# Kernel optimization log

Hardware: AMD Instinct MI355X
Metric: run time of the kernel (lower is better)

The kernel has to match this reference:

```python
import jax, jax.numpy as jnp
import numpy as np

B, S, DA, DV, DU, L, M = 16, 256, 1, 32, 1, 4, 12


def conv1x1(x, w, b):
    # x: [B,C,H,W], w: [O,C], b: [O]
    return jnp.einsum('bchw,oc->bohw', x, w) + b[None, :, None, None]


def setup_inputs() -> dict:
    key = jax.random.key(0)
    ks = jax.random.split(key, 12)
    sc = 0.02
    return {
        'x':    jax.random.normal(ks[0], (B, S, S, DA), dtype=jnp.float32),
        'p_w':  sc * jax.random.normal(ks[1], (DV, DA + 2), dtype=jnp.float32),
        'p_b':  sc * jax.random.normal(ks[2], (DV,), dtype=jnp.float32),
        'ws_w': sc * jax.random.normal(ks[3], (L, DV, DV), dtype=jnp.float32),
        'ws_b': sc * jax.random.normal(ks[4], (L, DV), dtype=jnp.float32),
        'w1r':  sc * jax.random.normal(ks[5], (L, DV, DV, M, M), dtype=jnp.float32),
        'w1i':  sc * jax.random.normal(ks[6], (L, DV, DV, M, M), dtype=jnp.float32),
        'w2r':  sc * jax.random.normal(ks[7], (L, DV, DV, M, M), dtype=jnp.float32),
        'w2i':  sc * jax.random.normal(ks[8], (L, DV, DV, M, M), dtype=jnp.float32),
        'q_w':  sc * jax.random.normal(ks[9], (DU, DV), dtype=jnp.float32),
        'q_b':  sc * jax.random.normal(ks[10], (DU,), dtype=jnp.float32),
    }


def fourier_layer(x, w1r, w1i, w2r, w2i):
    # x: [B,C,H,W]; FFT norm None == 'backward' (numpy/jax default)
    b, c, h, w = x.shape
    x_ft = jnp.fft.rfft2(x)                       # [B,C,H,W//2+1] complex
    W1 = w1r + 1j * w1i                           # [C,C,M,M]
    W2 = w2r + 1j * w2i
    top = jnp.einsum('bixy,ioxy->boxy', x_ft[:, :, :M, :M], W1)
    bot = jnp.einsum('bixy,ioxy->boxy', x_ft[:, :, -M:, :M], W2)
    out_ft = jnp.zeros((b, c, h, w // 2 + 1), dtype=x_ft.dtype)
    out_ft = out_ft.at[:, :, :M, :M].set(top)
    out_ft = out_ft.at[:, :, h - M:, :M].set(bot)
    return jnp.fft.irfft2(out_ft, s=(h, w))


def reference(x, p_w, p_b, ws_w, ws_b, w1r, w1i, w2r, w2i, q_w, q_b):
    b, sx, sy, _ = x.shape
    # grid as in get_grid (requires sx == sy, as the original implicitly does)
    gx = jnp.linspace(-1.0, 1.0, sx, dtype=jnp.float32)
    gy = jnp.linspace(-1.0, 1.0, sy, dtype=jnp.float32)
    gridx = jnp.broadcast_to(gx.reshape(1, 1, sx, 1), (b, sy, sx, 1))
    gridy = jnp.broadcast_to(gy.reshape(1, sy, 1, 1), (b, sy, sx, 1))
    grid = jnp.concatenate([gridy, gridx], axis=-1)     # [B,Sy,Sx,2]
    h = jnp.concatenate([x, grid], axis=-1)             # [B,S,S,DA+2]
    h = jnp.transpose(h, (0, 3, 1, 2))                  # NCHW
    h = conv1x1(h, p_w, p_b)                            # lifting
    for i in range(L):
        x1 = fourier_layer(h, w1r[i], w1i[i], w2r[i], w2i[i])
        x2 = conv1x1(h, ws_w[i], ws_b[i])
        h = x1 + x2
        if i < L - 1:
            h = jax.nn.relu(h)
    h = conv1x1(h, q_w, q_b)                            # projection -> [B,1,S,S]
    return jnp.transpose(h, (0, 2, 3, 1)).squeeze(-1)   # [B,S,S]
```

## Files before the change

### kernel.cpp

```cpp
#include <hip/hip_runtime.h>
#include <math.h>

#define NB 16
#define SS 256
#define DV 32
#define MM 12
#define MK 24
#define LL 4
#define TWO_PI_N 0.024543692606170259679f
#define TSTR 33

typedef float v2f __attribute__((ext_vector_type(2)));


__global__ __launch_bounds__(256) void k_prep(const float* __restrict__ ws_w,
        float* __restrict__ twT, float* __restrict__ wT, float* __restrict__ tw2)
{
    int j = threadIdx.x;
    #pragma unroll
    for (int k = 0; k < MM; ++k) {
        float ang = TWO_PI_N * (float)((k * j) & 255);
        float s, c; sincosf(ang, &s, &c);
        twT[j * (MM * 2) + 2 * k]     = c;
        twT[j * (MM * 2) + 2 * k + 1] = -s;
        tw2[(k * SS + j) * 2]     = c;
        tw2[(k * SS + j) * 2 + 1] = s;
    }
    for (int idx = threadIdx.x; idx < LL * DV * DV; idx += 256) {
        int l = idx >> 10, rem = idx & 1023, co = rem >> 5, ci = rem & 31;
        wT[(l * DV + ci) * DV + co] = ws_w[(l * DV + co) * DV + ci];
    }
}

__global__ __launch_bounds__(256) void k_lift(const float* __restrict__ x,
        const float* __restrict__ p_w, const float* __restrict__ p_b,
        float* __restrict__ h)
{
    int tid = threadIdx.x;
    int lane = tid & 63;
    int w = __builtin_amdgcn_readfirstlane(tid >> 6);
    int b  = blockIdx.x >> 6;
    int iy = ((blockIdx.x & 63) << 2) + w;
    int j0 = lane << 2;

    float4 xv = *(const float4*)(x + ((size_t)(b * SS + iy)) * SS + j0);
    float gy = -1.f + 2.f * (float)iy * (1.f / 255.f);
    float4 gx;
    gx.x = -1.f + 2.f * (float)j0 * (1.f / 255.f);
    gx.y = gx.x + 2.f / 255.f; gx.z = gx.y + 2.f / 255.f; gx.w = gx.z + 2.f / 255.f;

    float* hb = h + ((size_t)b * DV * SS + iy) * SS + j0;
    #pragma unroll
    for (int c = 0; c < DV; ++c) {
        float w0 = p_w[3*c], w1 = p_w[3*c+1], w2 = p_w[3*c+2], bb = p_b[c];
        float4 v;
        v.x = w0 * xv.x + w1 * gy + w2 * gx.x + bb;
        v.y = w0 * xv.y + w1 * gy + w2 * gx.y + bb;
        v.z = w0 * xv.z + w1 * gy + w2 * gx.z + bb;
        v.w = w0 * xv.w + w1 * gy + w2 * gx.w + bb;
        *(float4*)(hb + (size_t)c * SS * SS) = v;
    }
}

__global__ __launch_bounds__(512, 4) void k_rowdft(const float* __restrict__ h,
        const float* __restrict__ twT, float* __restrict__ A)
{
    __shared__ float smem[6336];
    int tid = threadIdx.x;
    int iy = tid & 127;
    int jq = __builtin_amdgcn_readfirstlane(tid >> 7);
    int bc = blockIdx.x >> 1;
    int iyh = blockIdx.x & 1;
    int b = bc >> 5, c = bc & 31;
    const float* hrow = h + (size_t)bc * SS * SS + (size_t)iyh * 128 * SS;

    v2f arai[MM];
    #pragma unroll
    for (int k = 0; k < MM; ++k) arai[k] = (v2f)(0.f);

    for (int t = 0; t < 8; ++t) {
        int jb = t * 32;
        __syncthreads();
        #pragma unroll
        for (int k = 0; k < 2; ++k) {
            int idx = tid + k * 512;
            int row = idx >> 3, col4 = idx & 7;
            float4 v = *(const float4*)(hrow + (size_t)row * SS + jb + col4 * 4);
            float* d = &smem[row * TSTR + col4 * 4];
            d[0] = v.x; d[1] = v.y; d[2] = v.z; d[3] = v.w;
        }
        __syncthreads();
        const float* rp = &smem[iy * TSTR + jq * 8];
        #pragma unroll
        for (int i = 0; i < 8; ++i) {
            float v = rp[i];
            const v2f* twj = (const v2f*)(twT + (size_t)(jb + jq * 8 + i) * (MM * 2));
            #pragma unroll
            for (int k = 0; k < MM; ++k)
                arai[k] += twj[k] * v;
        }
    }

    __syncthreads();
    if (jq & 1) {
        float* rd = &smem[(jq >> 1) * 3072];
        #pragma unroll
        for (int k = 0; k < MM; ++k) {
            rd[(2*k) * 128 + iy]     = arai[k].x;
            rd[(2*k + 1) * 128 + iy] = arai[k].y;
        }
    }
    __syncthreads();
    if (!(jq & 1)) {
        const float* rd = &smem[(jq >> 1) * 3072];
        #pragma unroll
        for (int k = 0; k < MM; ++k) {
            arai[k].x += rd[(2*k) * 128 + iy];
            arai[k].y += rd[(2*k + 1) * 128 + iy];
        }
    }
    __syncthreads();
    if (jq == 2) {
        #pragma unroll
        for (int k = 0; k < MM; ++k) {
            smem[(2*k) * 128 + iy]     = arai[k].x;
            smem[(2*k + 1) * 128 + iy] = arai[k].y;
        }
    }
    __syncthreads();
    if (jq == 0) {
        int iyg = iyh * 128 + iy;
        #pragma unroll
        for (int ky = 0; ky < MM; ++ky) {
            float2 val;
            val.x = arai[ky].x + smem[(2*ky) * 128 + iy];
            val.y = arai[ky].y + smem[(2*ky + 1) * 128 + iy];
            size_t o = ((((size_t)b * MM + ky) * DV + c) * SS + iyg) * 2;
            *(float2*)&A[o] = val;
        }
    }
}

__global__ __launch_bounds__(256, 4) void k_cm(const float* __restrict__ A,
        const float* __restrict__ w1r, const float* __restrict__ w1i,
        const float* __restrict__ w2r, const float* __restrict__ w2i,
        float* __restrict__ F, int l)
{
    __shared__ float FinS[DV][6][2];
    int blk = blockIdx.x;
    int mg = blk & 3;
    int bk = blk >> 2;
    int ky = bk % MM;
    int tid = threadIdx.x;
    int c = tid >> 3, ch = tid & 7;
    int iy0 = ch * 32;

    const float2* Ap = (const float2*)(A + ((size_t)bk * DV + c) * SS * 2);

    float fr[6], fi[6], pc[6], ps[6], sc[6], ssn[6];
    #pragma unroll
    for (int k = 0; k < 6; ++k) {
        int m = mg * 6 + k;
        int f = (m < MM) ? m : (232 + m);
        float s, cc;
        sincosf(TWO_PI_N * (float)f, &s, &cc);
        sc[k] = cc; ssn[k] = s;
        sincosf(TWO_PI_N * (float)((f * iy0) & 255), &s, &cc);
        pc[k] = cc; ps[k] = s;
        fr[k] = fi[k] = 0.f;
    }
    #pragma unroll 4
    for (int i = 0; i < 32; ++i) {
        float2 a = Ap[iy0 + i];
        #pragma unroll
        for (int k = 0; k < 6; ++k) {
            fr[k] += a.x * pc[k] + a.y * ps[k];
            fi[k] += a.y * pc[k] - a.x * ps[k];
            float np = pc[k] * sc[k] - ps[k] * ssn[k];
            float nq = pc[k] * ssn[k] + ps[k] * sc[k];
            pc[k] = np; ps[k] = nq;
        }
    }
    #pragma unroll
    for (int m = 1; m < 8; m <<= 1) {
        #pragma unroll
        for (int k = 0; k < 6; ++k) {
            fr[k] += __shfl_xor(fr[k], m, 64);
            fi[k] += __shfl_xor(fi[k], m, 64);
        }
    }
    #pragma unroll
    for (int k = 0; k < 6; ++k) {
        if (ch == k) { FinS[c][k][0] = fr[k]; FinS[c][k][1] = fi[k]; }
    }
    __syncthreads();

    if (ch < 6) {
        int o = c;
        int m = mg * 6 + ch;
        const float* Wr; const float* Wi; int xm;
        if (m < MM) { Wr = w1r; Wi = w1i; xm = m; }
        else        { Wr = w2r; Wi = w2i; xm = m - MM; }
        float scale = ((ky == 0) ? 1.0f : 2.0f) * (1.0f / 65536.0f);
        float orr = 0.f, oii = 0.f;
        #pragma unroll 4
        for (int i = 0; i < DV; ++i) {
            float gr = FinS[i][ch][0], gi = FinS[i][ch][1];
            size_t wi = ((size_t)(l * DV + i) * DV + o) * (MM * MM) + xm * MM + ky;
            float wr = Wr[wi], wim = Wi[wi];
            orr += gr * wr - gi * wim;
            oii += gr * wim + gi * wr;
        }
        size_t off = (((size_t)bk * MK + m) * DV + o) * 2;
        F[off] = orr * scale; F[off + 1] = oii * scale;
    }
}

__global__ __launch_bounds__(384) void k_inv1(const float* __restrict__ F,
        float* __restrict__ g)
{
    __shared__ float itw[MK * 2];
    int tid = threadIdx.x;
    int b = blockIdx.x >> 8, iy = blockIdx.x & 255;
    if (tid < MK) {
        int f = (tid < MM) ? tid : (232 + tid);
        float ang = TWO_PI_N * (float)((f * iy) & 255);
        float s, c; sincosf(ang, &s, &c);
        itw[2 * tid] = c; itw[2 * tid + 1] = s;
    }
    __syncthreads();

    int ky = tid >> 5, co = tid & 31;
    const float* Fp = F + ((size_t)(b * MM + ky) * MK) * (DV * 2) + 2 * co;
    float gr = 0.f, gi = 0.f;
    #pragma unroll
    for (int m = 0; m < MK; ++m) {
        float2 fv = *(const float2*)(Fp + (size_t)m * (DV * 2));
        float ic = itw[2 * m], is = itw[2 * m + 1];
        gr += fv.x * ic - fv.y * is;
        gi += fv.x * is + fv.y * ic;
    }
    size_t o = (((size_t)(b * SS + iy)) * MM + ky) * (DV * 2) + 2 * co;
    g[o] = gr; g[o + 1] = gi;
}

template<int FINAL>
__global__ __launch_bounds__(256, 4) void k_pt(float* __restrict__ h,
        const float* __restrict__ g, const float* __restrict__ wT,
        const float* __restrict__ ws_b, const float* __restrict__ tw2,
        const float* __restrict__ q_w, const float* __restrict__ q_b,
        float* __restrict__ out, int l)
{
    int tid = threadIdx.x;
    int lane = tid & 63;
    int w = __builtin_amdgcn_readfirstlane(tid >> 6);
    int b  = blockIdx.x >> 7;
    int iy = ((blockIdx.x & 127) << 1) + (w >> 1);
    int j0 = ((w & 1) << 7) + (lane << 1);

    float* hb = h + ((size_t)b * DV * SS + iy) * SS + j0;
    const float* wt  = wT + (size_t)l * DV * DV;
    const float* wsb = ws_b + (size_t)l * DV;

    float2 acc[DV];
    #pragma unroll
    for (int co = 0; co < DV; ++co) {
        float bv = wsb[co];
        acc[co].x = bv; acc[co].y = bv;
    }

    #pragma unroll 4
    for (int ci = 0; ci < DV; ++ci) {
        float2 hv = *(const float2*)(hb + (size_t)ci * SS * SS);
        const float* wc = wt + ci * DV;
        #pragma unroll
        for (int co = 0; co < DV; ++co) {
            float wv = wc[co];
            acc[co].x += wv * hv.x; acc[co].y += wv * hv.y;
        }
    }

    const float* gp = g + ((size_t)(b * SS + iy)) * (MM * DV * 2);
    #pragma unroll 2
    for (int ky = 0; ky < MM; ++ky) {
        float4 t4 = *(const float4*)(tw2 + ((size_t)ky * SS + j0) * 2);
        const float* Gk = gp + ky * (DV * 2);
        #pragma unroll
        for (int co = 0; co < DV; ++co) {
            float gr = Gk[2 * co], gi = Gk[2 * co + 1];
            acc[co].x += gr * t4.x - gi * t4.y;
            acc[co].y += gr * t4.z - gi * t4.w;
        }
    }

    if (FINAL) {
        float qb = q_b[0];
        float2 o2; o2.x = qb; o2.y = qb;
        #pragma unroll
        for (int co = 0; co < DV; ++co) {
            float qv = q_w[co];
            o2.x += qv * acc[co].x; o2.y += qv * acc[co].y;
        }
        *(float2*)(out + ((size_t)(b * SS + iy)) * SS + j0) = o2;
    } else {
        #pragma unroll
        for (int co = 0; co < DV; ++co) {
            float2 v;
            v.x = fmaxf(acc[co].x, 0.f); v.y = fmaxf(acc[co].y, 0.f);
            *(float2*)(hb + (size_t)co * SS * SS) = v;
        }
    }
}

extern "C" void kernel_launch(void* const* d_in, const int* in_sizes, int n_in,
                              void* d_out, int out_size, void* d_ws, size_t ws_size,
                              hipStream_t stream)
{
    const float* x    = (const float*)d_in[0];
    const float* p_w  = (const float*)d_in[1];
    const float* p_b  = (const float*)d_in[2];
    const float* ws_w = (const float*)d_in[3];
    const float* ws_b = (const float*)d_in[4];
    const float* w1r  = (const float*)d_in[5];
    const float* w1i  = (const float*)d_in[6];
    const float* w2r  = (const float*)d_in[7];
    const float* w2i  = (const float*)d_in[8];
    const float* q_w  = (const float*)d_in[9];
    const float* q_b  = (const float*)d_in[10];
    float* out = (float*)d_out;

    float* h   = (float*)d_ws;
    float* A   = h   + (size_t)NB * DV * SS * SS;
    float* F   = A   + (size_t)NB * MM * DV * SS * 2;
    float* g   = F   + (size_t)NB * MM * MK * DV * 2;
    float* twT = g   + (size_t)NB * SS * MM * DV * 2;
    float* wT  = twT + (size_t)SS * MM * 2;
    float* tw2 = wT  + (size_t)LL * DV * DV;

    dim3 blk(256);
    k_prep<<<1, blk, 0, stream>>>(ws_w, twT, wT, tw2);
    k_lift<<<NB * 64, blk, 0, stream>>>(x, p_w, p_b, h);
    for (int l = 0; l < LL; ++l) {
        k_rowdft<<<NB * DV * 2, dim3(512), 0, stream>>>(h, twT, A);
        k_cm<<<NB * MM * 4, blk, 0, stream>>>(A, w1r, w1i, w2r, w2i, F, l);
        k_inv1<<<NB * SS, dim3(384), 0, stream>>>(F, g);
        if (l < LL - 1)
            k_pt<0><<<NB * 128, blk, 0, stream>>>(h, g, wT, ws_b, tw2,
                                                  nullptr, nullptr, nullptr, l);
        else
            k_pt<1><<<NB * 128, blk, 0, stream>>>(h, g, wT, ws_b, tw2,
                                                  q_w, q_b, out, l);
    }
}
```

Baseline: 698.8 us.

## Fuse row DFT into lifting and pointwise kernels via LDS-resident rows

The lifting and the non-final pointwise/ReLU kernels now keep each computed h row (all 32 channels) in LDS and immediately compute the truncated row DFT from it. Results are reduced across segments in LDS and written to A. This removes the separate row-DFT kernel and its full re-read of h from global memory for each layer. The cost is that the fused kernels use larger LDS allocations and a different thread mapping, which may lower occupancy and change how efficient the pointwise stage is.

```diff
diff --git a/kernel.cpp b/kernel.cpp
--- a/kernel.cpp
+++ b/kernel.cpp
@@ -8,7 +8,7 @@
 #define MK 24
 #define LL 4
 #define TWO_PI_N 0.024543692606170259679f
-#define TSTR 33
+#define HSTR 257
 
 typedef float v2f __attribute__((ext_vector_type(2)));
 
@@ -32,113 +32,127 @@
     }
 }
 
-__global__ __launch_bounds__(256) void k_lift(const float* __restrict__ x,
+__device__ __forceinline__ void row_dft_from_lds(float* smem,
+        const float* __restrict__ twT, float* __restrict__ A,
+        int b, int iy, int tid)
+{
+    int c   = tid & 31;
+    int seg = tid >> 5;
+    int j0  = seg << 5;
+
+    v2f arai[MM];
+    #pragma unroll
+    for (int k = 0; k < MM; ++k) arai[k] = (v2f)(0.f);
+
+    const float* hp = smem + c * HSTR + j0;
+    #pragma unroll 2
+    for (int i = 0; i < 32; ++i) {
+        float v = hp[i];
+        const float4* twj = (const float4*)(twT + (size_t)(j0 + i) * (MM * 2));
+        #pragma unroll
+        for (int kk = 0; kk < 6; ++kk) {
+            float4 t = twj[kk];
+            v2f t0; t0.x = t.x; t0.y = t.y;
+            v2f t1; t1.x = t.z; t1.y = t.w;
+            arai[2 * kk]     += t0 * v;
+            arai[2 * kk + 1] += t1 * v;
+        }
+    }
+
+    __syncthreads();
+    v2f* red = (v2f*)smem;
+    #pragma unroll
+    for (int k = 0; k < MM; ++k) red[tid * 13 + k] = arai[k];
+    __syncthreads();
+
+    #pragma unroll
+    for (int rep = 0; rep < 2; ++rep) {
+        int o = tid + rep * 256;
+        if (o < 384) {
+            int k = o >> 5, cc = o & 31;
+            v2f s = (v2f)(0.f);
+            #pragma unroll
+            for (int sg = 0; sg < 8; ++sg)
+                s += red[(sg * 32 + cc) * 13 + k];
+            size_t off = ((((size_t)b * MM + k) * DV + cc) * SS + iy) * 2;
+            A[off]     = s.x;
+            A[off + 1] = s.y;
+        }
+    }
+}
+
+__global__ __launch_bounds__(256, 4) void k_liftdft(const float* __restrict__ x,
         const float* __restrict__ p_w, const float* __restrict__ p_b,
-        float* __restrict__ h)
-{
-    int tid = threadIdx.x;
-    int lane = tid & 63;
-    int w = __builtin_amdgcn_readfirstlane(tid >> 6);
-    int b  = blockIdx.x >> 6;
-    int iy = ((blockIdx.x & 63) << 2) + w;
-    int j0 = lane << 2;
-
-    float4 xv = *(const float4*)(x + ((size_t)(b * SS + iy)) * SS + j0);
+        float* __restrict__ h, const float* __restrict__ twT, float* __restrict__ A)
+{
+    __shared__ float smem[DV * HSTR];
+    int tid = threadIdx.x;
+    int b  = blockIdx.x >> 8;
+    int iy = blockIdx.x & 255;
+    int j  = tid;
+
+    float xv = x[((size_t)(b * SS + iy)) * SS + j];
     float gy = -1.f + 2.f * (float)iy * (1.f / 255.f);
-    float4 gx;
-    gx.x = -1.f + 2.f * (float)j0 * (1.f / 255.f);
-    gx.y = gx.x + 2.f / 255.f; gx.z = gx.y + 2.f / 255.f; gx.w = gx.z + 2.f / 255.f;
-
-    float* hb = h + ((size_t)b * DV * SS + iy) * SS + j0;
+    float gx = -1.f + 2.f * (float)j  * (1.f / 255.f);
+
+    float* hb = h + ((size_t)b * DV * SS + iy) * SS + j;
     #pragma unroll
     for (int c = 0; c < DV; ++c) {
-        float w0 = p_w[3*c], w1 = p_w[3*c+1], w2 = p_w[3*c+2], bb = p_b[c];
-        float4 v;
-        v.x = w0 * xv.x + w1 * gy + w2 * gx.x + bb;
-        v.y = w0 * xv.y + w1 * gy + w2 * gx.y + bb;
-        v.z = w0 * xv.z + w1 * gy + w2 * gx.z + bb;
-        v.w = w0 * xv.w + w1 * gy + w2 * gx.w + bb;
-        *(float4*)(hb + (size_t)c * SS * SS) = v;
-    }
-}
-
-__global__ __launch_bounds__(512, 4) void k_rowdft(const float* __restrict__ h,
-        const float* __restrict__ twT, float* __restrict__ A)
-{
-    __shared__ float smem[6336];
-    int tid = threadIdx.x;
-    int iy = tid & 127;
-    int jq = __builtin_amdgcn_readfirstlane(tid >> 7);
-    int bc = blockIdx.x >> 1;
-    int iyh = blockIdx.x & 1;
-    int b = bc >> 5, c = bc & 31;
-    const float* hrow = h + (size_t)bc * SS * SS + (size_t)iyh * 128 * SS;
-
-    v2f arai[MM];
-    #pragma unroll
-    for (int k = 0; k < MM; ++k) arai[k] = (v2f)(0.f);
-
-    for (int t = 0; t < 8; ++t) {
-        int jb = t * 32;
-        __syncthreads();
-        #pragma unroll
-        for (int k = 0; k < 2; ++k) {
-            int idx = tid + k * 512;
-            int row = idx >> 3, col4 = idx & 7;
-            float4 v = *(const float4*)(hrow + (size_t)row * SS + jb + col4 * 4);
-            float* d = &smem[row * TSTR + col4 * 4];
-            d[0] = v.x; d[1] = v.y; d[2] = v.z; d[3] = v.w;
-        }
-        __syncthreads();
-        const float* rp = &smem[iy * TSTR + jq * 8];
-        #pragma unroll
-        for (int i = 0; i < 8; ++i) {
-            float v = rp[i];
-            const v2f* twj = (const v2f*)(twT + (size_t)(jb + jq * 8 + i) * (MM * 2));
-            #pragma unroll
-            for (int k = 0; k < MM; ++k)
-                arai[k] += twj[k] * v;
-        }
-    }
-
-    __syncthreads();
-    if (jq & 1) {
-        float* rd = &smem[(jq >> 1) * 3072];
-        #pragma unroll
-        for (int k = 0; k < MM; ++k) {
-            rd[(2*k) * 128 + iy]     = arai[k].x;
-            rd[(2*k + 1) * 128 + iy] = arai[k].y;
-        }
-    }
-    __syncthreads();
-    if (!(jq & 1)) {
-        const float* rd = &smem[(jq >> 1) * 3072];
-        #pragma unroll
-        for (int k = 0; k < MM; ++k) {
-            arai[k].x += rd[(2*k) * 128 + iy];
-            arai[k].y += rd[(2*k + 1) * 128 + iy];
-        }
-    }
-    __syncthreads();
-    if (jq == 2) {
-        #pragma unroll
-        for (int k = 0; k < MM; ++k) {
-            smem[(2*k) * 128 + iy]     = arai[k].x;
-            smem[(2*k + 1) * 128 + iy] = arai[k].y;
-        }
-    }
-    __syncthreads();
-    if (jq == 0) {
-        int iyg = iyh * 128 + iy;
-        #pragma unroll
-        for (int ky = 0; ky < MM; ++ky) {
-            float2 val;
-            val.x = arai[ky].x + smem[(2*ky) * 128 + iy];
-            val.y = arai[ky].y + smem[(2*ky + 1) * 128 + iy];
-            size_t o = ((((size_t)b * MM + ky) * DV + c) * SS + iyg) * 2;
-            *(float2*)&A[o] = val;
-        }
-    }
+        float v = p_w[3*c] * xv + p_w[3*c+1] * gy + p_w[3*c+2] * gx + p_b[c];
+        *(hb + (size_t)c * SS * SS) = v;
+        smem[c * HSTR + j] = v;
+    }
+    __syncthreads();
+    row_dft_from_lds(smem, twT, A, b, iy, tid);
+}
+
+__global__ __launch_bounds__(256, 4) void k_ptdft(float* __restrict__ h,
+        const float* __restrict__ g, const float* __restrict__ wT,
+        const float* __restrict__ ws_b, const float* __restrict__ tw2,
+        const float* __restrict__ twT, float* __restrict__ A, int l)
+{
+    __shared__ float smem[DV * HSTR];
+    int tid = threadIdx.x;
+    int b  = blockIdx.x >> 8;
+    int iy = blockIdx.x & 255;
+    int j  = tid;
+
+    float* hb = h + ((size_t)b * DV * SS + iy) * SS + j;
+    const float* wt  = wT + (size_t)l * DV * DV;
+    const float* wsb = ws_b + (size_t)l * DV;
+
+    float acc[DV];
+    #pragma unroll
+    for (int co = 0; co < DV; ++co) acc[co] = wsb[co];
+
+    #pragma unroll 4
+    for (int ci = 0; ci < DV; ++ci) {
+        float hv = *(hb + (size_t)ci * SS * SS);
+        const float* wc = wt + ci * DV;
+        #pragma unroll
+        for (int co = 0; co < DV; ++co) acc[co] += wc[co] * hv;
+    }
+
+    const float* gp = g + ((size_t)(b * SS + iy)) * (MM * DV * 2);
+    #pragma unroll 2
+    for (int ky = 0; ky < MM; ++ky) {
+        float2 t2 = *(const float2*)(tw2 + ((size_t)ky * SS + j) * 2);
+        const float* Gk = gp + ky * (DV * 2);
+        #pragma unroll
+        for (int co = 0; co < DV; ++co) {
+            float gr = Gk[2 * co], gi = Gk[2 * co + 1];
+            acc[co] += gr * t2.x - gi * t2.y;
+        }
+    }
+
+    #pragma unroll
+    for (int co = 0; co < DV; ++co) {
+        float v = fmaxf(acc[co], 0.f);
+        *(hb + (size_t)co * SS * SS) = v;
+        smem[co * HSTR + j] = v;
+    }
+    __syncthreads();
+    row_dft_from_lds(smem, twT, A, b, iy, tid);
 }
 
 __global__ __launch_bounds__(256, 4) void k_cm(const float* __restrict__ A,
@@ -339,14 +353,12 @@
 
     dim3 blk(256);
     k_prep<<<1, blk, 0, stream>>>(ws_w, twT, wT, tw2);
-    k_lift<<<NB * 64, blk, 0, stream>>>(x, p_w, p_b, h);
+    k_liftdft<<<NB * SS, blk, 0, stream>>>(x, p_w, p_b, h, twT, A);
     for (int l = 0; l < LL; ++l) {
-        k_rowdft<<<NB * DV * 2, dim3(512), 0, stream>>>(h, twT, A);
         k_cm<<<NB * MM * 4, blk, 0, stream>>>(A, w1r, w1i, w2r, w2i, F, l);
         k_inv1<<<NB * SS, dim3(384), 0, stream>>>(F, g);
         if (l < LL - 1)
-            k_pt<0><<<NB * 128, blk, 0, stream>>>(h, g, wT, ws_b, tw2,
-                                                  nullptr, nullptr, nullptr, l);
+            k_ptdft<<<NB * SS, blk, 0, stream>>>(h, g, wT, ws_b, tw2, twT, A, l);
         else
             k_pt<1><<<NB * 128, blk, 0, stream>>>(h, g, wT, ws_b, tw2,
                                                   q_w, q_b, out, l);
```

Result: slower. 917.1 us (+31.2%).
